# Optimization experiments

Hardware: AMD Instinct MI355X
Metric: run time of the kernel (lower is better)

Reference implementation:

```python
import jax, jax.numpy as jnp
import numpy as np

EMBED = 1024
HEADS = 16
HEAD_DIM = EMBED // HEADS
WIN = 256  # attention_window w; band width = 2w+1


def setup_inputs() -> dict:
    key = jax.random.key(0)
    ks = jax.random.split(key, 10)
    b, s, e = 2, 4096, EMBED
    scale = 1.0 / np.sqrt(e)
    inp = {"x": jax.random.normal(ks[0], (b, s, e), jnp.float32)}
    for i, (wn, bn) in enumerate([("Wq", "bq"), ("Wk", "bk"), ("Wv", "bv"), ("Wo", "bo")]):
        inp[wn] = jax.random.normal(ks[1 + i], (e, e), jnp.float32) * scale
        inp[bn] = jax.random.normal(ks[5 + i], (e,), jnp.float32) * 0.01
    return inp


def _rope_headaxis(x):
    # Replicates RotaryEmbedding applied to [b, s, h, d]: the original indexes
    # x.shape[2] (== num_heads here), so phase varies over the HEAD axis.
    h, d = x.shape[2], x.shape[3]
    inv = 1.0 / (10000.0 ** (jnp.arange(0, d, 2, dtype=jnp.float32) / d))
    freqs = jnp.arange(h, dtype=jnp.float32)[:, None] * inv[None, :]
    emb = jnp.concatenate([freqs, freqs], axis=-1)  # [h, d]
    cos = jnp.cos(emb)[None, None]  # [1,1,h,d]
    sin = jnp.sin(emb)[None, None]
    x2 = jnp.stack([-x[..., 1::2], x[..., 0::2]], axis=-1).reshape(x.shape)
    return x * cos + x2 * sin


def reference(x, Wq, bq, Wk, bk, Wv, bv, Wo, bo):
    b, s, e = x.shape
    h, d, w = HEADS, HEAD_DIM, WIN
    q = (x @ Wq.T + bq).reshape(b, s, h, d)
    k = (x @ Wk.T + bk).reshape(b, s, h, d)
    v = (x @ Wv.T + bv).reshape(b, s, h, d)
    q = _rope_headaxis(q) / jnp.sqrt(jnp.float32(d))
    k = _rope_headaxis(k)

    # Band (sliding-window) attention: query chunk c of size w attends to key
    # chunks c-1, c, c+1 (3w keys); relative-position + boundary masking makes
    # this identical to the original sliding_chunks band of width 2w+1.
    nc = s // w
    qc = q.reshape(b, nc, w, h, d)
    pad = [(0, 0), (w, w), (0, 0), (0, 0)]
    kp = jnp.pad(k, pad)
    vp = jnp.pad(v, pad)
    idx = jnp.arange(nc)[:, None] * w + jnp.arange(3 * w)[None, :]  # [nc, 3w]
    k3 = kp[:, idx]  # [b, nc, 3w, h, d]
    v3 = vp[:, idx]
    scores = jnp.einsum('bcxhd,bcyhd->bhcxy', qc, k3)  # [b,h,nc,w,3w]

    c = jnp.arange(nc)[:, None, None]
    xq = jnp.arange(w)[None, :, None]
    y = jnp.arange(3 * w)[None, None, :]
    kpos = c * w + y - w  # absolute key position
    valid = (y >= xq) & (y <= xq + 2 * w) & (kpos >= 0) & (kpos < s)
    scores = jnp.where(valid[None, None], scores, -jnp.inf)

    probs = jax.nn.softmax(scores, axis=-1)  # fp32 softmax, as in original
    ctx = jnp.einsum('bhcxy,bcyhd->bcxhd', probs, v3).reshape(b, s, e)
    return ctx @ Wo.T + bo
```

## Files before the change

### kernel.cpp

```cpp
#include <hip/hip_runtime.h>


typedef _Float16 half8 __attribute__((ext_vector_type(8)));
typedef _Float16 half4v __attribute__((ext_vector_type(4)));
typedef float floatx4 __attribute__((ext_vector_type(4)));

typedef __attribute__((address_space(3))) unsigned int lds_u32;
typedef const __attribute__((address_space(1))) unsigned int glb_u32;

__device__ __forceinline__ void async_copy16(const void* g, void* l) {
  __builtin_amdgcn_global_load_lds((glb_u32*)g, (lds_u32*)l, 16, 0, 0);
}

__global__ __launch_bounds__(256) void convert_kernel(
    const float* __restrict__ x, const float* __restrict__ wq,
    const float* __restrict__ wk, const float* __restrict__ wv,
    const float* __restrict__ wo, _Float16* __restrict__ dst) {
  const int e0 = (blockIdx.x * 256 + threadIdx.x) * 4;
  const float* src; int off;
  if      (e0 <  8388608) { src = x;  off = e0; }
  else if (e0 <  9437184) { src = wq; off = e0 -  8388608; }
  else if (e0 < 10485760) { src = wk; off = e0 -  9437184; }
  else if (e0 < 11534336) { src = wv; off = e0 - 10485760; }
  else                    { src = wo; off = e0 - 11534336; }
  const float4 f = *(const float4*)(src + off);
  half4v h;
  h[0] = (_Float16)f.x; h[1] = (_Float16)f.y;
  h[2] = (_Float16)f.z; h[3] = (_Float16)f.w;
  *(half4v*)(dst + e0) = h;
}

__global__ __launch_bounds__(256, 2) void gemm_qkv_kernel(
    const _Float16* __restrict__ A, const _Float16* __restrict__ w0,
    const _Float16* __restrict__ w1, const _Float16* __restrict__ w2,
    const float* __restrict__ b0, const float* __restrict__ b1,
    const float* __restrict__ b2, _Float16* __restrict__ o0,
    _Float16* __restrict__ o1, _Float16* __restrict__ o2) {
  __shared__ _Float16 smem[17408];
  _Float16* As = smem;
  _Float16* Bs = smem + 8192;

  const int tid = threadIdx.x;
  const int w = tid >> 6, lane = tid & 63;
  const int l4 = lane & 15, quad = lane >> 4;
  const int wm = w & 1, wn = w >> 1;

  const int bid = blockIdx.x;
  const int xcd = bid & 7, li = bid >> 3;
  const int z = li >> 6, r_ = li & 63;
  const int n_l = r_ >> 3, m_l = r_ & 7;
  const int m0 = (xcd * 8 + m_l) * 128;
  const int n0 = n_l * 128;

  const _Float16* B; const float* bias; _Float16* out;
  if (z == 0)      { B = w0; bias = b0; out = o0; }
  else if (z == 1) { B = w1; bias = b1; out = o1; }
  else             { B = w2; bias = b2; out = o2; }
  const bool dorope = z < 2;
  const float scl = (z == 0) ? 0.18033688f : 1.0f;

  const floatx4 zero = {0.f, 0.f, 0.f, 0.f};
  floatx4 acc[4][4];
#pragma unroll
  for (int i = 0; i < 4; ++i)
#pragma unroll
    for (int j = 0; j < 4; ++j) acc[i][j] = zero;

  for (int kt = 0; kt < 16; ++kt) {
    const int k0 = kt * 64;
#pragma unroll
    for (int i = 0; i < 4; ++i) {
      const int p = i * 256 + tid;
      const int r = p >> 3;
      const int c = (p & 7) ^ (r & 7);
      async_copy16(A + (m0 + r) * 1024 + k0 + c * 8, As + (i * 256 + w * 64) * 8);
      async_copy16(B + (n0 + r) * 1024 + k0 + c * 8, Bs + (i * 256 + w * 64) * 8);
    }
    __syncthreads();
#pragma unroll
    for (int ks = 0; ks < 2; ++ks) {
      half8 af[4], bf[4];
#pragma unroll
      for (int mt = 0; mt < 4; ++mt)
        af[mt] = *(const half8*)(As + (wm * 64 + mt * 16 + l4) * 64 +
                                 (((ks * 4 + quad) ^ (l4 & 7)) * 8));
#pragma unroll
      for (int nt = 0; nt < 4; ++nt)
        bf[nt] = *(const half8*)(Bs + (wn * 64 + nt * 16 + l4) * 64 +
                                 (((ks * 4 + quad) ^ (l4 & 7)) * 8));
#pragma unroll
      for (int mt = 0; mt < 4; ++mt)
#pragma unroll
        for (int nt = 0; nt < 4; ++nt)
          acc[mt][nt] = __builtin_amdgcn_mfma_f32_16x16x32_f16(af[mt], bf[nt], acc[mt][nt], 0, 0, 0);
    }
    __syncthreads();
  }

  _Float16* tile = smem;
#pragma unroll
  for (int nt = 0; nt < 4; ++nt) {
    const int n = n0 + wn * 64 + nt * 16 + l4;
    const float bval = bias[n];
    const int hh = n >> 6;
    float c_ = 1.f, ss = 0.f;
    if (dorope) {
      const float freq = __expf((float)(n & 31) * -0.28782314f);
      float s_;
      __sincosf((float)hh * freq, &s_, &c_);
      ss = (n & 1) ? s_ : -s_;
    }
#pragma unroll
    for (int mt = 0; mt < 4; ++mt)
#pragma unroll
      for (int r = 0; r < 4; ++r) {
        float val = acc[mt][nt][r] + bval;
        const float prt = __shfl_xor(val, 1);
        if (dorope) val = (val * c_ + prt * ss) * scl;
        const int ml = wm * 64 + mt * 16 + quad * 4 + r;
        const int nl = wn * 64 + nt * 16 + l4;
        if (z == 2) tile[nl * 132 + ml] = (_Float16)val;
        else        tile[ml * 132 + nl] = (_Float16)val;
      }
  }
  __syncthreads();
  if (z == 2) {
#pragma unroll
    for (int j = 0; j < 8; ++j) {
      const int idx = j * 256 + tid;
      const int row = idx >> 4, cb = idx & 15;
      const int n = n0 + row, hh = n >> 6, dd = n & 63;
      const int m = m0 + cb * 8, bb = m >> 12, s = m & 4095;
      const half8 vals = *(const half8*)(tile + row * 132 + cb * 8);
      *(half8*)(out + (bb * 16 + hh) * 262144 + dd * 4096 + s) = vals;
    }
  } else {
#pragma unroll
    for (int j = 0; j < 8; ++j) {
      const int idx = j * 256 + tid;
      const int row = idx >> 4, cb = idx & 15;
      const int n = n0 + cb * 8, hh = n >> 6, dd = n & 63;
      const int m = m0 + row, bb = m >> 12, s = m & 4095;
      const half8 vals = *(const half8*)(tile + row * 132 + cb * 8);
      *(half8*)(out + ((bb * 16 + hh) * 4096 + s) * 64 + dd) = vals;
    }
  }
}

__global__ __launch_bounds__(256, 2) void gemm_out_kernel(
    const _Float16* __restrict__ A, const _Float16* __restrict__ B,
    const float* __restrict__ bias, float* __restrict__ out) {
  __shared__ _Float16 smem[16384];
  _Float16* As = smem;
  _Float16* Bs = smem + 8192;

  const int tid = threadIdx.x;
  const int w = tid >> 6, lane = tid & 63;
  const int l4 = lane & 15, quad = lane >> 4;
  const int wm = w & 1, wn = w >> 1;

  const int bid = blockIdx.x;
  const int xcd = bid & 7, li = bid >> 3;
  const int n_l = li >> 3, m_l = li & 7;
  const int m0 = (xcd * 8 + m_l) * 128;
  const int n0 = n_l * 128;

  const floatx4 zero = {0.f, 0.f, 0.f, 0.f};
  floatx4 acc[4][4];
#pragma unroll
  for (int i = 0; i < 4; ++i)
#pragma unroll
    for (int j = 0; j < 4; ++j) acc[i][j] = zero;

  for (int kt = 0; kt < 16; ++kt) {
    const int k0 = kt * 64;
#pragma unroll
    for (int i = 0; i < 4; ++i) {
      const int p = i * 256 + tid;
      const int r = p >> 3;
      const int c = (p & 7) ^ (r & 7);
      async_copy16(A + (m0 + r) * 1024 + k0 + c * 8, As + (i * 256 + w * 64) * 8);
      async_copy16(B + (n0 + r) * 1024 + k0 + c * 8, Bs + (i * 256 + w * 64) * 8);
    }
    __syncthreads();
#pragma unroll
    for (int ks = 0; ks < 2; ++ks) {
      half8 af[4], bf[4];
#pragma unroll
      for (int mt = 0; mt < 4; ++mt)
        af[mt] = *(const half8*)(As + (wm * 64 + mt * 16 + l4) * 64 +
                                 (((ks * 4 + quad) ^ (l4 & 7)) * 8));
#pragma unroll
      for (int nt = 0; nt < 4; ++nt)
        bf[nt] = *(const half8*)(Bs + (wn * 64 + nt * 16 + l4) * 64 +
                                 (((ks * 4 + quad) ^ (l4 & 7)) * 8));
#pragma unroll
      for (int mt = 0; mt < 4; ++mt)
#pragma unroll
        for (int nt = 0; nt < 4; ++nt)
          acc[mt][nt] = __builtin_amdgcn_mfma_f32_16x16x32_f16(af[mt], bf[nt], acc[mt][nt], 0, 0, 0);
    }
    __syncthreads();
  }

#pragma unroll
  for (int nt = 0; nt < 4; ++nt) {
    const int n = n0 + wn * 64 + nt * 16 + l4;
    const float bval = bias[n];
#pragma unroll
    for (int mt = 0; mt < 4; ++mt)
#pragma unroll
      for (int r = 0; r < 4; ++r) {
        const int m = m0 + wm * 64 + mt * 16 + quad * 4 + r;
        out[m * 1024 + n] = acc[mt][nt][r] + bval;
      }
  }
}

__global__ __launch_bounds__(256, 2) void attn_kernel(
    const _Float16* __restrict__ qg, const _Float16* __restrict__ kg,
    const _Float16* __restrict__ vtg, _Float16* __restrict__ ctx) {
  __shared__ _Float16 Ks[2][128 * 64];
  __shared__ _Float16 Vs[2][64 * 128];

  const int tid = threadIdx.x;
  const int w = tid >> 6, lane = tid & 63;
  const int l4 = lane & 15, quad = lane >> 4;

  const int bid = blockIdx.x;
  const int xcd = bid & 7, li = bid >> 3;
  const int bh = xcd * 4 + (li >> 4);
  const int q0 = (li & 15) * 256;

  const _Float16* qbh = qg + bh * 262144;
  const _Float16* kbh = kg + bh * 262144;
  const _Float16* vbh = vtg + bh * 262144;

  half8 qf[2][2][2];
#pragma unroll
  for (int sub = 0; sub < 2; ++sub)
#pragma unroll
    for (int nt = 0; nt < 2; ++nt)
#pragma unroll
      for (int ks = 0; ks < 2; ++ks)
        qf[sub][nt][ks] = *(const half8*)(qbh + (q0 + sub * 128 + w * 32 + nt * 16 + l4) * 64 +
                                          ks * 32 + quad * 8);

  const floatx4 zero = {0.f, 0.f, 0.f, 0.f};
  floatx4 OT[2][4][2];
  float l_st[2][2];
#pragma unroll
  for (int sub = 0; sub < 2; ++sub) {
#pragma unroll
    for (int md = 0; md < 4; ++md)
#pragma unroll
      for (int nt = 0; nt < 2; ++nt) OT[sub][md][nt] = zero;
#pragma unroll
    for (int nt = 0; nt < 2; ++nt) l_st[sub][nt] = 0.f;
  }

  const int tb = (q0 == 0) ? 2 : 0;
  const int te = (q0 == 3840) ? 3 : 5;

  auto stage = [&](int b_, int kv0_) {
#pragma unroll
    for (int i = 0; i < 4; ++i) {
      const int p = i * 256 + tid;
      const int rk = p >> 3, ck = (p & 7) ^ (rk & 7);
      async_copy16(kbh + (kv0_ + rk) * 64 + ck * 8, &Ks[b_][(i * 256 + w * 64) * 8]);
      const int rv = p >> 4, cv = (p & 15) ^ (rv & 7);
      async_copy16(vbh + rv * 4096 + kv0_ + cv * 8, &Vs[b_][(i * 256 + w * 64) * 8]);
    }
  };

  stage(tb & 1, q0 - 256 + tb * 128);

  for (int t = tb; t <= te; ++t) {
    const int kv0 = q0 - 256 + t * 128;
    if (t < te) {
      stage((t + 1) & 1, kv0 + 128);
      asm volatile("s_waitcnt vmcnt(8)" ::: "memory");
    } else {
      asm volatile("s_waitcnt vmcnt(0)" ::: "memory");
    }
    __builtin_amdgcn_s_barrier();
    const _Float16* Kc = Ks[t & 1];
    const _Float16* Vc = Vs[t & 1];

#pragma unroll
    for (int sub = 0; sub < 2; ++sub) {
      const int qbase = q0 + sub * 128 + w * 32;
#pragma unroll
      for (int hf = 0; hf < 2; ++hf) {
        const int kb = hf * 64;
        const int k_lo = kv0 + kb, k_hi = k_lo + 63;
        if (k_lo - (qbase + 31) > 256 || k_hi - qbase < -256) continue;
        const bool needm = (k_lo - (qbase + 31) < -256) || (k_hi - qbase > 256);

        floatx4 ST[4][2];
#pragma unroll
        for (int m = 0; m < 4; ++m)
#pragma unroll
          for (int nt = 0; nt < 2; ++nt) ST[m][nt] = zero;
#pragma unroll
        for (int ks = 0; ks < 2; ++ks)
#pragma unroll
          for (int m = 0; m < 4; ++m) {
            const half8 kf = *(const half8*)(Kc + (kb + m * 16 + l4) * 64 +
                                             ((ks * 4 + quad) ^ (l4 & 7)) * 8);
#pragma unroll
            for (int nt = 0; nt < 2; ++nt)
              ST[m][nt] = __builtin_amdgcn_mfma_f32_16x16x32_f16(kf, qf[sub][nt][ks], ST[m][nt], 0, 0, 0);
          }

        if (needm) {
#pragma unroll
          for (int m = 0; m < 4; ++m)
#pragma unroll
            for (int r = 0; r < 4; ++r) {
              const int key = kv0 + kb + m * 16 + quad * 4 + r;
#pragma unroll
              for (int nt = 0; nt < 2; ++nt) {
                const int d = key - (qbase + nt * 16 + l4);
                if (d < -256 || d > 256) ST[m][nt][r] = -1e30f;
              }
            }
        }

#pragma unroll
        for (int nt = 0; nt < 2; ++nt) {
          float rs = 0.f;
#pragma unroll
          for (int m = 0; m < 4; ++m)
#pragma unroll
            for (int r = 0; r < 4; ++r) {
              const float pv = exp2f(ST[m][nt][r] - 4.0f);
              ST[m][nt][r] = pv;
              rs += pv;
            }
          l_st[sub][nt] += rs;
        }

#pragma unroll
        for (int m = 0; m < 4; ++m) {
          half4v pb[2];
#pragma unroll
          for (int nt = 0; nt < 2; ++nt) {
            const auto lo = __builtin_amdgcn_cvt_pkrtz(ST[m][nt][0], ST[m][nt][1]);
            const auto hi = __builtin_amdgcn_cvt_pkrtz(ST[m][nt][2], ST[m][nt][3]);
            pb[nt][0] = (_Float16)lo[0]; pb[nt][1] = (_Float16)lo[1];
            pb[nt][2] = (_Float16)hi[0]; pb[nt][3] = (_Float16)hi[1];
          }
#pragma unroll
          for (int md = 0; md < 4; ++md) {
            const half4v vf = *(const half4v*)(Vc + (md * 16 + l4) * 128 +
                                               (((hf * 8 + m * 2 + (quad >> 1)) ^ (l4 & 7)) * 8 +
                                                (quad & 1) * 4));
#pragma unroll
            for (int nt = 0; nt < 2; ++nt)
              OT[sub][md][nt] = __builtin_amdgcn_mfma_f32_16x16x16f16(vf, pb[nt], OT[sub][md][nt], 0, 0, 0);
          }
        }
      }
    }

    if (t < te) {
      asm volatile("s_waitcnt lgkmcnt(0)" ::: "memory");
      __builtin_amdgcn_sched_barrier(0);
      __builtin_amdgcn_s_barrier();
    }
  }

  const int b = bh >> 4, hh = bh & 15;
#pragma unroll
  for (int sub = 0; sub < 2; ++sub)
#pragma unroll
    for (int nt = 0; nt < 2; ++nt) {
      float lt = l_st[sub][nt];
      lt += __shfl_xor(lt, 16);
      lt += __shfl_xor(lt, 32);
      const float inv_l = 1.f / lt;
      const int s = q0 + sub * 128 + w * 32 + nt * 16 + l4;
#pragma unroll
      for (int md = 0; md < 4; ++md) {
        half4v o;
#pragma unroll
        for (int r = 0; r < 4; ++r) o[r] = (_Float16)(OT[sub][md][nt][r] * inv_l);
        *(half4v*)(ctx + (b * 4096 + s) * 1024 + hh * 64 + md * 16 + quad * 4) = o;
      }
    }
}

extern "C" void kernel_launch(void* const* d_in, const int* in_sizes, int n_in,
                              void* d_out, int out_size, void* d_ws, size_t ws_size,
                              hipStream_t stream) {
  const float* x  = (const float*)d_in[0];
  const float* Wq = (const float*)d_in[1];
  const float* bq = (const float*)d_in[2];
  const float* Wk = (const float*)d_in[3];
  const float* bk = (const float*)d_in[4];
  const float* Wv = (const float*)d_in[5];
  const float* bv = (const float*)d_in[6];
  const float* Wo = (const float*)d_in[7];
  const float* bo = (const float*)d_in[8];

  _Float16* ws   = (_Float16*)d_ws;
  _Float16* xh   = ws;
  _Float16* wqh  = ws + 8388608;
  _Float16* wkh  = ws + 9437184;
  _Float16* wvh  = ws + 10485760;
  _Float16* woh  = ws + 11534336;
  _Float16* qh   = ws + 12582912;
  _Float16* kh   = ws + 20971520;
  _Float16* vth  = ws + 29360128;
  _Float16* ctxh = xh;

  convert_kernel<<<12288, 256, 0, stream>>>(x, Wq, Wk, Wv, Wo, ws);
  gemm_qkv_kernel<<<1536, 256, 0, stream>>>(xh, wqh, wkh, wvh,
                                            bq, bk, bv, qh, kh, vth);
  attn_kernel<<<512, 256, 0, stream>>>(qh, kh, vth, ctxh);
  gemm_out_kernel<<<512, 256, 0, stream>>>(ctxh, woh, bo, (float*)d_out);
}
```

Measured before the change: 227.9 us.

## Double-buffer GEMM K-tiles with async LDS prefetch in QKV and output projections

Both projection GEMMs now use two LDS buffers with a K-tile of 32 instead of a single buffer with a K-tile of 64. The next tile's global-to-LDS async copies are issued before computing the current one, and a partial vmcnt wait lets loads overlap the MFMA work. The swizzle is adjusted for the narrower 32-wide rows, and per-thread offsets are hoisted out of the loop. In exchange the loop runs twice as many iterations with two barriers each, and each iteration does less MFMA work per barrier.

```diff
diff --git a/kernel.cpp b/kernel.cpp
--- a/kernel.cpp
+++ b/kernel.cpp
@@ -37,8 +37,6 @@
     const float* __restrict__ b2, _Float16* __restrict__ o0,
     _Float16* __restrict__ o1, _Float16* __restrict__ o2) {
   __shared__ _Float16 smem[17408];
-  _Float16* As = smem;
-  _Float16* Bs = smem + 8192;
 
   const int tid = threadIdx.x;
   const int w = tid >> 6, lane = tid & 63;
@@ -59,6 +57,28 @@
   const bool dorope = z < 2;
   const float scl = (z == 0) ? 0.18033688f : 1.0f;
 
+  int aoff[2], boff[2];
+#pragma unroll
+  for (int i = 0; i < 2; ++i) {
+    const int p = i * 256 + tid;
+    const int r = p >> 2;
+    const int c = (p & 3) ^ (r & 3) ^ ((r >> 2) & 1);
+    aoff[i] = (m0 + r) * 1024 + c * 8;
+    boff[i] = (n0 + r) * 1024 + c * 8;
+  }
+  const int ldst = w * 512;
+
+  auto stage = [&](int b_, int kt) {
+    _Float16* Ad = smem + b_ * 8192;
+    _Float16* Bd = Ad + 4096;
+    const int k0 = kt * 32;
+#pragma unroll
+    for (int i = 0; i < 2; ++i) {
+      async_copy16(A + aoff[i] + k0, Ad + i * 2048 + ldst);
+      async_copy16(B + boff[i] + k0, Bd + i * 2048 + ldst);
+    }
+  };
+
   const floatx4 zero = {0.f, 0.f, 0.f, 0.f};
   floatx4 acc[4][4];
 #pragma unroll
@@ -66,35 +86,34 @@
 #pragma unroll
     for (int j = 0; j < 4; ++j) acc[i][j] = zero;
 
-  for (int kt = 0; kt < 16; ++kt) {
-    const int k0 = kt * 64;
-#pragma unroll
-    for (int i = 0; i < 4; ++i) {
-      const int p = i * 256 + tid;
-      const int r = p >> 3;
-      const int c = (p & 7) ^ (r & 7);
-      async_copy16(A + (m0 + r) * 1024 + k0 + c * 8, As + (i * 256 + w * 64) * 8);
-      async_copy16(B + (n0 + r) * 1024 + k0 + c * 8, Bs + (i * 256 + w * 64) * 8);
-    }
-    __syncthreads();
-#pragma unroll
-    for (int ks = 0; ks < 2; ++ks) {
-      half8 af[4], bf[4];
-#pragma unroll
-      for (int mt = 0; mt < 4; ++mt)
-        af[mt] = *(const half8*)(As + (wm * 64 + mt * 16 + l4) * 64 +
-                                 (((ks * 4 + quad) ^ (l4 & 7)) * 8));
+  const int slot = (quad ^ (l4 & 3) ^ ((l4 >> 2) & 1)) * 8;
+
+  stage(0, 0);
+  for (int kt = 0; kt < 32; ++kt) {
+    if (kt < 31) {
+      stage((kt + 1) & 1, kt + 1);
+      asm volatile("s_waitcnt vmcnt(4)" ::: "memory");
+    } else {
+      asm volatile("s_waitcnt vmcnt(0)" ::: "memory");
+    }
+    __builtin_amdgcn_s_barrier();
+    const _Float16* As = smem + (kt & 1) * 8192;
+    const _Float16* Bs = As + 4096;
+    half8 af[4], bf[4];
+#pragma unroll
+    for (int mt = 0; mt < 4; ++mt)
+      af[mt] = *(const half8*)(As + (wm * 64 + mt * 16 + l4) * 32 + slot);
+#pragma unroll
+    for (int nt = 0; nt < 4; ++nt)
+      bf[nt] = *(const half8*)(Bs + (wn * 64 + nt * 16 + l4) * 32 + slot);
+#pragma unroll
+    for (int mt = 0; mt < 4; ++mt)
 #pragma unroll
       for (int nt = 0; nt < 4; ++nt)
-        bf[nt] = *(const half8*)(Bs + (wn * 64 + nt * 16 + l4) * 64 +
-                                 (((ks * 4 + quad) ^ (l4 & 7)) * 8));
-#pragma unroll
-      for (int mt = 0; mt < 4; ++mt)
-#pragma unroll
-        for (int nt = 0; nt < 4; ++nt)
-          acc[mt][nt] = __builtin_amdgcn_mfma_f32_16x16x32_f16(af[mt], bf[nt], acc[mt][nt], 0, 0, 0);
-    }
-    __syncthreads();
+        acc[mt][nt] = __builtin_amdgcn_mfma_f32_16x16x32_f16(af[mt], bf[nt], acc[mt][nt], 0, 0, 0);
+    asm volatile("s_waitcnt lgkmcnt(0)" ::: "memory");
+    __builtin_amdgcn_sched_barrier(0);
+    __builtin_amdgcn_s_barrier();
   }
 
   _Float16* tile = smem;
@@ -151,8 +170,6 @@
     const _Float16* __restrict__ A, const _Float16* __restrict__ B,
     const float* __restrict__ bias, float* __restrict__ out) {
   __shared__ _Float16 smem[16384];
-  _Float16* As = smem;
-  _Float16* Bs = smem + 8192;
 
   const int tid = threadIdx.x;
   const int w = tid >> 6, lane = tid & 63;
@@ -165,6 +182,28 @@
   const int m0 = (xcd * 8 + m_l) * 128;
   const int n0 = n_l * 128;
 
+  int aoff[2], boff[2];
+#pragma unroll
+  for (int i = 0; i < 2; ++i) {
+    const int p = i * 256 + tid;
+    const int r = p >> 2;
+    const int c = (p & 3) ^ (r & 3) ^ ((r >> 2) & 1);
+    aoff[i] = (m0 + r) * 1024 + c * 8;
+    boff[i] = (n0 + r) * 1024 + c * 8;
+  }
+  const int ldst = w * 512;
+
+  auto stage = [&](int b_, int kt) {
+    _Float16* Ad = smem + b_ * 8192;
+    _Float16* Bd = Ad + 4096;
+    const int k0 = kt * 32;
+#pragma unroll
+    for (int i = 0; i < 2; ++i) {
+      async_copy16(A + aoff[i] + k0, Ad + i * 2048 + ldst);
+      async_copy16(B + boff[i] + k0, Bd + i * 2048 + ldst);
+    }
+  };
+
   const floatx4 zero = {0.f, 0.f, 0.f, 0.f};
   floatx4 acc[4][4];
 #pragma unroll
@@ -172,35 +211,34 @@
 #pragma unroll
     for (int j = 0; j < 4; ++j) acc[i][j] = zero;
 
-  for (int kt = 0; kt < 16; ++kt) {
-    const int k0 = kt * 64;
-#pragma unroll
-    for (int i = 0; i < 4; ++i) {
-      const int p = i * 256 + tid;
-      const int r = p >> 3;
-      const int c = (p & 7) ^ (r & 7);
-      async_copy16(A + (m0 + r) * 1024 + k0 + c * 8, As + (i * 256 + w * 64) * 8);
-      async_copy16(B + (n0 + r) * 1024 + k0 + c * 8, Bs + (i * 256 + w * 64) * 8);
-    }
-    __syncthreads();
-#pragma unroll
-    for (int ks = 0; ks < 2; ++ks) {
-      half8 af[4], bf[4];
-#pragma unroll
-      for (int mt = 0; mt < 4; ++mt)
-        af[mt] = *(const half8*)(As + (wm * 64 + mt * 16 + l4) * 64 +
-                                 (((ks * 4 + quad) ^ (l4 & 7)) * 8));
+  const int slot = (quad ^ (l4 & 3) ^ ((l4 >> 2) & 1)) * 8;
+
+  stage(0, 0);
+  for (int kt = 0; kt < 32; ++kt) {
+    if (kt < 31) {
+      stage((kt + 1) & 1, kt + 1);
+      asm volatile("s_waitcnt vmcnt(4)" ::: "memory");
+    } else {
+      asm volatile("s_waitcnt vmcnt(0)" ::: "memory");
+    }
+    __builtin_amdgcn_s_barrier();
+    const _Float16* As = smem + (kt & 1) * 8192;
+    const _Float16* Bs = As + 4096;
+    half8 af[4], bf[4];
+#pragma unroll
+    for (int mt = 0; mt < 4; ++mt)
+      af[mt] = *(const half8*)(As + (wm * 64 + mt * 16 + l4) * 32 + slot);
+#pragma unroll
+    for (int nt = 0; nt < 4; ++nt)
+      bf[nt] = *(const half8*)(Bs + (wn * 64 + nt * 16 + l4) * 32 + slot);
+#pragma unroll
+    for (int mt = 0; mt < 4; ++mt)
 #pragma unroll
       for (int nt = 0; nt < 4; ++nt)
-        bf[nt] = *(const half8*)(Bs + (wn * 64 + nt * 16 + l4) * 64 +
-                                 (((ks * 4 + quad) ^ (l4 & 7)) * 8));
-#pragma unroll
-      for (int mt = 0; mt < 4; ++mt)
-#pragma unroll
-        for (int nt = 0; nt < 4; ++nt)
-          acc[mt][nt] = __builtin_amdgcn_mfma_f32_16x16x32_f16(af[mt], bf[nt], acc[mt][nt], 0, 0, 0);
-    }
-    __syncthreads();
+        acc[mt][nt] = __builtin_amdgcn_mfma_f32_16x16x32_f16(af[mt], bf[nt], acc[mt][nt], 0, 0, 0);
+    asm volatile("s_waitcnt lgkmcnt(0)" ::: "memory");
+    __builtin_amdgcn_sched_barrier(0);
+    __builtin_amdgcn_s_barrier();
   }
 
 #pragma unroll
```

New measurement: 236.1 us. 1.04x slower.

## Double-buffer LDS tiles in QKV and output GEMMs with async prefetch

Applied to the files above, without the earlier changes.

Both GEMM kernels now use two LDS buffers. Each iteration issues the global-to-LDS async copies for the next K tile before computing on the current one, and waits with a partial vmcnt so loads overlap the MFMAs. Address offsets are precomputed once per thread, and __syncthreads is replaced by explicit waitcnt plus s_barrier. LDS per block grows to 64KB, which could limit occupancy at two blocks per CU, and the hand-written waitcnt counts must match the number of outstanding loads.

```diff
diff --git a/kernel.cpp b/kernel.cpp
--- a/kernel.cpp
+++ b/kernel.cpp
@@ -36,9 +36,7 @@
     const float* __restrict__ b0, const float* __restrict__ b1,
     const float* __restrict__ b2, _Float16* __restrict__ o0,
     _Float16* __restrict__ o1, _Float16* __restrict__ o2) {
-  __shared__ _Float16 smem[17408];
-  _Float16* As = smem;
-  _Float16* Bs = smem + 8192;
+  __shared__ _Float16 smem[32768];
 
   const int tid = threadIdx.x;
   const int w = tid >> 6, lane = tid & 63;
@@ -59,6 +57,28 @@
   const bool dorope = z < 2;
   const float scl = (z == 0) ? 0.18033688f : 1.0f;
 
+  int aoff[4], boff[4];
+#pragma unroll
+  for (int i = 0; i < 4; ++i) {
+    const int p = i * 256 + tid;
+    const int r = p >> 3;
+    const int c = (p & 7) ^ (r & 7);
+    aoff[i] = (m0 + r) * 1024 + c * 8;
+    boff[i] = (n0 + r) * 1024 + c * 8;
+  }
+  const int ldst = (w * 64) * 8;
+
+  auto stage = [&](int b_, int kt) {
+    _Float16* Ad = smem + b_ * 16384;
+    _Float16* Bd = Ad + 8192;
+    const int k0 = kt * 64;
+#pragma unroll
+    for (int i = 0; i < 4; ++i) {
+      async_copy16(A + aoff[i] + k0, Ad + i * 2048 + ldst);
+      async_copy16(B + boff[i] + k0, Bd + i * 2048 + ldst);
+    }
+  };
+
   const floatx4 zero = {0.f, 0.f, 0.f, 0.f};
   floatx4 acc[4][4];
 #pragma unroll
@@ -66,17 +86,17 @@
 #pragma unroll
     for (int j = 0; j < 4; ++j) acc[i][j] = zero;
 
+  stage(0, 0);
   for (int kt = 0; kt < 16; ++kt) {
-    const int k0 = kt * 64;
-#pragma unroll
-    for (int i = 0; i < 4; ++i) {
-      const int p = i * 256 + tid;
-      const int r = p >> 3;
-      const int c = (p & 7) ^ (r & 7);
-      async_copy16(A + (m0 + r) * 1024 + k0 + c * 8, As + (i * 256 + w * 64) * 8);
-      async_copy16(B + (n0 + r) * 1024 + k0 + c * 8, Bs + (i * 256 + w * 64) * 8);
-    }
-    __syncthreads();
+    if (kt < 15) {
+      stage((kt + 1) & 1, kt + 1);
+      asm volatile("s_waitcnt vmcnt(8)" ::: "memory");
+    } else {
+      asm volatile("s_waitcnt vmcnt(0)" ::: "memory");
+    }
+    __builtin_amdgcn_s_barrier();
+    const _Float16* As = smem + (kt & 1) * 16384;
+    const _Float16* Bs = As + 8192;
 #pragma unroll
     for (int ks = 0; ks < 2; ++ks) {
       half8 af[4], bf[4];
@@ -94,7 +114,9 @@
         for (int nt = 0; nt < 4; ++nt)
           acc[mt][nt] = __builtin_amdgcn_mfma_f32_16x16x32_f16(af[mt], bf[nt], acc[mt][nt], 0, 0, 0);
     }
-    __syncthreads();
+    asm volatile("s_waitcnt lgkmcnt(0)" ::: "memory");
+    __builtin_amdgcn_sched_barrier(0);
+    __builtin_amdgcn_s_barrier();
   }
 
   _Float16* tile = smem;
@@ -150,9 +172,7 @@
 __global__ __launch_bounds__(256, 2) void gemm_out_kernel(
     const _Float16* __restrict__ A, const _Float16* __restrict__ B,
     const float* __restrict__ bias, float* __restrict__ out) {
-  __shared__ _Float16 smem[16384];
-  _Float16* As = smem;
-  _Float16* Bs = smem + 8192;
+  __shared__ _Float16 smem[32768];
 
   const int tid = threadIdx.x;
   const int w = tid >> 6, lane = tid & 63;
@@ -165,6 +185,28 @@
   const int m0 = (xcd * 8 + m_l) * 128;
   const int n0 = n_l * 128;
 
+  int aoff[4], boff[4];
+#pragma unroll
+  for (int i = 0; i < 4; ++i) {
+    const int p = i * 256 + tid;
+    const int r = p >> 3;
+    const int c = (p & 7) ^ (r & 7);
+    aoff[i] = (m0 + r) * 1024 + c * 8;
+    boff[i] = (n0 + r) * 1024 + c * 8;
+  }
+  const int ldst = (w * 64) * 8;
+
+  auto stage = [&](int b_, int kt) {
+    _Float16* Ad = smem + b_ * 16384;
+    _Float16* Bd = Ad + 8192;
+    const int k0 = kt * 64;
+#pragma unroll
+    for (int i = 0; i < 4; ++i) {
+      async_copy16(A + aoff[i] + k0, Ad + i * 2048 + ldst);
+      async_copy16(B + boff[i] + k0, Bd + i * 2048 + ldst);
+    }
+  };
+
   const floatx4 zero = {0.f, 0.f, 0.f, 0.f};
   floatx4 acc[4][4];
 #pragma unroll
@@ -172,17 +214,17 @@
 #pragma unroll
     for (int j = 0; j < 4; ++j) acc[i][j] = zero;
 
+  stage(0, 0);
   for (int kt = 0; kt < 16; ++kt) {
-    const int k0 = kt * 64;
-#pragma unroll
-    for (int i = 0; i < 4; ++i) {
-      const int p = i * 256 + tid;
-      const int r = p >> 3;
-      const int c = (p & 7) ^ (r & 7);
-      async_copy16(A + (m0 + r) * 1024 + k0 + c * 8, As + (i * 256 + w * 64) * 8);
-      async_copy16(B + (n0 + r) * 1024 + k0 + c * 8, Bs + (i * 256 + w * 64) * 8);
-    }
-    __syncthreads();
+    if (kt < 15) {
+      stage((kt + 1) & 1, kt + 1);
+      asm volatile("s_waitcnt vmcnt(8)" ::: "memory");
+    } else {
+      asm volatile("s_waitcnt vmcnt(0)" ::: "memory");
+    }
+    __builtin_amdgcn_s_barrier();
+    const _Float16* As = smem + (kt & 1) * 16384;
+    const _Float16* Bs = As + 8192;
 #pragma unroll
     for (int ks = 0; ks < 2; ++ks) {
       half8 af[4], bf[4];
@@ -200,7 +242,9 @@
         for (int nt = 0; nt < 4; ++nt)
           acc[mt][nt] = __builtin_amdgcn_mfma_f32_16x16x32_f16(af[mt], bf[nt], acc[mt][nt], 0, 0, 0);
     }
-    __syncthreads();
+    asm volatile("s_waitcnt lgkmcnt(0)" ::: "memory");
+    __builtin_amdgcn_sched_barrier(0);
+    __builtin_amdgcn_s_barrier();
   }
 
 #pragma unroll
```

Result: slower. 233.9 us (+2.6%).

## Use 256x128 tiles with 8 waves and a triple-buffered async GEMM mainloop

Applied to the files above, without the earlier changes.

Both GEMMs now share a mainloop with 512-thread blocks computing 256x128 tiles and three LDS stages. Global-to-LDS async copies for tile k+2 are interleaved with the MFMA work, using explicit vmcnt waits, barriers and raised wave priority around the MFMAs. The goal is to hide memory latency and cut per-K-step sync overhead compared with the single-buffered load-sync-compute loop. In exchange each block uses 144KB of LDS, so occupancy drops to one block per CU, and the QKV epilogue now writes its tile in two halves.

```diff
diff --git a/kernel.cpp b/kernel.cpp
--- a/kernel.cpp
+++ b/kernel.cpp
@@ -30,27 +30,121 @@
   *(half4v*)(dst + e0) = h;
 }
 
-__global__ __launch_bounds__(256, 2) void gemm_qkv_kernel(
+__device__ __forceinline__ void mainloop_8ph(
+    const _Float16* __restrict__ A, const _Float16* __restrict__ B,
+    _Float16* smem, const int m0, const int n0, floatx4 (&acc)[4][4]) {
+  const int tid = threadIdx.x;
+  const int w = tid >> 6, lane = tid & 63;
+  const int l4 = lane & 15, quad = lane >> 4;
+  const int wm = w >> 1, wn = w & 1;
+
+  int asrc[4], bsrc[2];
+#pragma unroll
+  for (int i = 0; i < 4; ++i) {
+    const int p = i * 512 + tid;
+    const int r = p >> 3, c = (p & 7) ^ (r & 7);
+    asrc[i] = (m0 + r) * 1024 + c * 8;
+  }
+#pragma unroll
+  for (int i = 0; i < 2; ++i) {
+    const int p = i * 512 + tid;
+    const int r = p >> 3, c = (p & 7) ^ (r & 7);
+    bsrc[i] = (n0 + r) * 1024 + c * 8;
+  }
+  const int dl = w * 512;
+
+  const int arow = (wm * 64 + l4) * 64;
+  const int brow = (wn * 64 + l4) * 64;
+
+#pragma unroll
+  for (int i = 0; i < 4; ++i)
+#pragma unroll
+    for (int j = 0; j < 4; ++j) acc[i][j] = (floatx4){0.f, 0.f, 0.f, 0.f};
+
+  auto stage_full = [&](int bufbase, int kt) {
+    _Float16* Ad = smem + bufbase;
+    _Float16* Bd = Ad + 16384;
+    const int k0 = kt * 64;
+#pragma unroll
+    for (int i = 0; i < 4; ++i) async_copy16(A + asrc[i] + k0, Ad + i * 4096 + dl);
+#pragma unroll
+    for (int i = 0; i < 2; ++i) async_copy16(B + bsrc[i] + k0, Bd + i * 4096 + dl);
+  };
+
+  stage_full(0, 0);
+  stage_full(24576, 1);
+  asm volatile("s_waitcnt vmcnt(6)" ::: "memory");
+  __builtin_amdgcn_s_barrier();
+
+  int cb = 0, pb = 49152;
+  for (int T = 0; T < 16; ++T) {
+    const _Float16* As = smem + cb;
+    const _Float16* Bs = As + 16384;
+    const bool pf = (T + 2) < 16;
+    _Float16* Ad = smem + pb;
+    _Float16* Bd = Ad + 16384;
+    const int k2 = (T + 2) * 64;
+
+#pragma unroll
+    for (int ks = 0; ks < 2; ++ks) {
+      half8 af[4], bf[4];
+      const int ch = ((ks * 4 + quad) ^ (l4 & 7)) * 8;
+#pragma unroll
+      for (int mt = 0; mt < 4; ++mt)
+        af[mt] = *(const half8*)(As + arow + mt * 1024 + ch);
+#pragma unroll
+      for (int nt = 0; nt < 4; ++nt)
+        bf[nt] = *(const half8*)(Bs + brow + nt * 1024 + ch);
+      if (pf) {
+        if (ks == 0) {
+          async_copy16(A + asrc[0] + k2, Ad + dl);
+          async_copy16(A + asrc[1] + k2, Ad + 4096 + dl);
+          async_copy16(B + bsrc[0] + k2, Bd + dl);
+        } else {
+          async_copy16(A + asrc[2] + k2, Ad + 8192 + dl);
+          async_copy16(A + asrc[3] + k2, Ad + 12288 + dl);
+          async_copy16(B + bsrc[1] + k2, Bd + 4096 + dl);
+        }
+      }
+      __builtin_amdgcn_s_barrier();
+      asm volatile("s_waitcnt lgkmcnt(0)" ::: "memory");
+      __builtin_amdgcn_sched_barrier(0);
+      __builtin_amdgcn_s_setprio(1);
+#pragma unroll
+      for (int mt = 0; mt < 4; ++mt)
+#pragma unroll
+        for (int nt = 0; nt < 4; ++nt)
+          acc[mt][nt] = __builtin_amdgcn_mfma_f32_16x16x32_f16(af[mt], bf[nt], acc[mt][nt], 0, 0, 0);
+      __builtin_amdgcn_s_setprio(0);
+      if (ks == 1) {
+        if (T < 14) asm volatile("s_waitcnt vmcnt(6)" ::: "memory");
+        else        asm volatile("s_waitcnt vmcnt(0)" ::: "memory");
+      }
+      __builtin_amdgcn_s_barrier();
+    }
+    cb += 24576; if (cb == 73728) cb = 0;
+    pb += 24576; if (pb == 73728) pb = 0;
+  }
+}
+
+__global__ __launch_bounds__(512) void gemm_qkv_kernel(
     const _Float16* __restrict__ A, const _Float16* __restrict__ w0,
     const _Float16* __restrict__ w1, const _Float16* __restrict__ w2,
     const float* __restrict__ b0, const float* __restrict__ b1,
     const float* __restrict__ b2, _Float16* __restrict__ o0,
     _Float16* __restrict__ o1, _Float16* __restrict__ o2) {
-  __shared__ _Float16 smem[17408];
-  _Float16* As = smem;
-  _Float16* Bs = smem + 8192;
+  __shared__ _Float16 smem[73728];
 
   const int tid = threadIdx.x;
   const int w = tid >> 6, lane = tid & 63;
   const int l4 = lane & 15, quad = lane >> 4;
-  const int wm = w & 1, wn = w >> 1;
+  const int wm = w >> 1, wn = w & 1;
 
   const int bid = blockIdx.x;
   const int xcd = bid & 7, li = bid >> 3;
-  const int z = li >> 6, r_ = li & 63;
-  const int n_l = r_ >> 3, m_l = r_ & 7;
-  const int m0 = (xcd * 8 + m_l) * 128;
-  const int n0 = n_l * 128;
+  const int z = li >> 5, r_ = li & 31;
+  const int m0 = (xcd * 4 + (r_ & 3)) * 256;
+  const int n0 = (r_ >> 2) * 128;
 
   const _Float16* B; const float* bias; _Float16* out;
   if (z == 0)      { B = w0; bias = b0; out = o0; }
@@ -59,149 +153,83 @@
   const bool dorope = z < 2;
   const float scl = (z == 0) ? 0.18033688f : 1.0f;
 
-  const floatx4 zero = {0.f, 0.f, 0.f, 0.f};
   floatx4 acc[4][4];
-#pragma unroll
-  for (int i = 0; i < 4; ++i)
-#pragma unroll
-    for (int j = 0; j < 4; ++j) acc[i][j] = zero;
-
-  for (int kt = 0; kt < 16; ++kt) {
-    const int k0 = kt * 64;
-#pragma unroll
-    for (int i = 0; i < 4; ++i) {
-      const int p = i * 256 + tid;
-      const int r = p >> 3;
-      const int c = (p & 7) ^ (r & 7);
-      async_copy16(A + (m0 + r) * 1024 + k0 + c * 8, As + (i * 256 + w * 64) * 8);
-      async_copy16(B + (n0 + r) * 1024 + k0 + c * 8, Bs + (i * 256 + w * 64) * 8);
+  mainloop_8ph(A, B, smem, m0, n0, acc);
+
+  _Float16* tile = smem;
+  for (int h = 0; h < 2; ++h) {
+    if ((wm >> 1) == h) {
+#pragma unroll
+      for (int nt = 0; nt < 4; ++nt) {
+        const int n = n0 + wn * 64 + nt * 16 + l4;
+        const float bval = bias[n];
+        const int hh = n >> 6;
+        float c_ = 1.f, ss = 0.f;
+        if (dorope) {
+          const float freq = __expf((float)(n & 31) * -0.28782314f);
+          float s_;
+          __sincosf((float)hh * freq, &s_, &c_);
+          ss = (n & 1) ? s_ : -s_;
+        }
+#pragma unroll
+        for (int mt = 0; mt < 4; ++mt)
+#pragma unroll
+          for (int r = 0; r < 4; ++r) {
+            float val = acc[mt][nt][r] + bval;
+            const float prt = __shfl_xor(val, 1);
+            if (dorope) val = (val * c_ + prt * ss) * scl;
+            const int ml = (wm & 1) * 64 + mt * 16 + quad * 4 + r;
+            const int nl = wn * 64 + nt * 16 + l4;
+            if (z == 2) tile[nl * 132 + ml] = (_Float16)val;
+            else        tile[ml * 132 + nl] = (_Float16)val;
+          }
+      }
     }
     __syncthreads();
-#pragma unroll
-    for (int ks = 0; ks < 2; ++ks) {
-      half8 af[4], bf[4];
-#pragma unroll
-      for (int mt = 0; mt < 4; ++mt)
-        af[mt] = *(const half8*)(As + (wm * 64 + mt * 16 + l4) * 64 +
-                                 (((ks * 4 + quad) ^ (l4 & 7)) * 8));
-#pragma unroll
-      for (int nt = 0; nt < 4; ++nt)
-        bf[nt] = *(const half8*)(Bs + (wn * 64 + nt * 16 + l4) * 64 +
-                                 (((ks * 4 + quad) ^ (l4 & 7)) * 8));
-#pragma unroll
-      for (int mt = 0; mt < 4; ++mt)
-#pragma unroll
-        for (int nt = 0; nt < 4; ++nt)
-          acc[mt][nt] = __builtin_amdgcn_mfma_f32_16x16x32_f16(af[mt], bf[nt], acc[mt][nt], 0, 0, 0);
+    const int mg = m0 + h * 128;
+    const int bb = mg >> 12, sg = mg & 4095;
+    if (z == 2) {
+#pragma unroll
+      for (int j = 0; j < 4; ++j) {
+        const int idx = j * 512 + tid;
+        const int row = idx >> 4, cbk = idx & 15;
+        const int n = n0 + row, hh = n >> 6, dd = n & 63;
+        const int s = sg + cbk * 8;
+        const half8 vals = *(const half8*)(tile + row * 132 + cbk * 8);
+        *(half8*)(out + (bb * 16 + hh) * 262144 + dd * 4096 + s) = vals;
+      }
+    } else {
+#pragma unroll
+      for (int j = 0; j < 4; ++j) {
+        const int idx = j * 512 + tid;
+        const int row = idx >> 4, cbk = idx & 15;
+        const int n = n0 + cbk * 8, hh = n >> 6, dd = n & 63;
+        const int s = sg + row;
+        const half8 vals = *(const half8*)(tile + row * 132 + cbk * 8);
+        *(half8*)(out + ((bb * 16 + hh) * 4096 + s) * 64 + dd) = vals;
+      }
     }
     __syncthreads();
   }
-
-  _Float16* tile = smem;
-#pragma unroll
-  for (int nt = 0; nt < 4; ++nt) {
-    const int n = n0 + wn * 64 + nt * 16 + l4;
-    const float bval = bias[n];
-    const int hh = n >> 6;
-    float c_ = 1.f, ss = 0.f;
-    if (dorope) {
-      const float freq = __expf((float)(n & 31) * -0.28782314f);
-      float s_;
-      __sincosf((float)hh * freq, &s_, &c_);
-      ss = (n & 1) ? s_ : -s_;
-    }
-#pragma unroll
-    for (int mt = 0; mt < 4; ++mt)
-#pragma unroll
-      for (int r = 0; r < 4; ++r) {
-        float val = acc[mt][nt][r] + bval;
-        const float prt = __shfl_xor(val, 1);
-        if (dorope) val = (val * c_ + prt * ss) * scl;
-        const int ml = wm * 64 + mt * 16 + quad * 4 + r;
-        const int nl = wn * 64 + nt * 16 + l4;
-        if (z == 2) tile[nl * 132 + ml] = (_Float16)val;
-        else        tile[ml * 132 + nl] = (_Float16)val;
-      }
-  }
-  __syncthreads();
-  if (z == 2) {
-#pragma unroll
-    for (int j = 0; j < 8; ++j) {
-      const int idx = j * 256 + tid;
-      const int row = idx >> 4, cb = idx & 15;
-      const int n = n0 + row, hh = n >> 6, dd = n & 63;
-      const int m = m0 + cb * 8, bb = m >> 12, s = m & 4095;
-      const half8 vals = *(const half8*)(tile + row * 132 + cb * 8);
-      *(half8*)(out + (bb * 16 + hh) * 262144 + dd * 4096 + s) = vals;
-    }
-  } else {
-#pragma unroll
-    for (int j = 0; j < 8; ++j) {
-      const int idx = j * 256 + tid;
-      const int row = idx >> 4, cb = idx & 15;
-      const int n = n0 + cb * 8, hh = n >> 6, dd = n & 63;
-      const int m = m0 + row, bb = m >> 12, s = m & 4095;
-      const half8 vals = *(const half8*)(tile + row * 132 + cb * 8);
-      *(half8*)(out + ((bb * 16 + hh) * 4096 + s) * 64 + dd) = vals;
-    }
-  }
-}
-
-__global__ __launch_bounds__(256, 2) void gemm_out_kernel(
+}
+
+__global__ __launch_bounds__(512) void gemm_out_kernel(
     const _Float16* __restrict__ A, const _Float16* __restrict__ B,
     const float* __restrict__ bias, float* __restrict__ out) {
-  __shared__ _Float16 smem[16384];
-  _Float16* As = smem;
-  _Float16* Bs = smem + 8192;
+  __shared__ _Float16 smem[73728];
 
   const int tid = threadIdx.x;
   const int w = tid >> 6, lane = tid & 63;
   const int l4 = lane & 15, quad = lane >> 4;
-  const int wm = w & 1, wn = w >> 1;
+  const int wm = w >> 1, wn = w & 1;
 
   const int bid = blockIdx.x;
   const int xcd = bid & 7, li = bid >> 3;
-  const int n_l = li >> 3, m_l = li & 7;
-  const int m0 = (xcd * 8 + m_l) * 128;
-  const int n0 = n_l * 128;
-
-  const floatx4 zero = {0.f, 0.f, 0.f, 0.f};
+  const int m0 = (xcd * 4 + (li & 3)) * 256;
+  const int n0 = (li >> 2) * 128;
+
   floatx4 acc[4][4];
-#pragma unroll
-  for (int i = 0; i < 4; ++i)
-#pragma unroll
-    for (int j = 0; j < 4; ++j) acc[i][j] = zero;
-
-  for (int kt = 0; kt < 16; ++kt) {
-    const int k0 = kt * 64;
-#pragma unroll
-    for (int i = 0; i < 4; ++i) {
-      const int p = i * 256 + tid;
-      const int r = p >> 3;
-      const int c = (p & 7) ^ (r & 7);
-      async_copy16(A + (m0 + r) * 1024 + k0 + c * 8, As + (i * 256 + w * 64) * 8);
-      async_copy16(B + (n0 + r) * 1024 + k0 + c * 8, Bs + (i * 256 + w * 64) * 8);
-    }
-    __syncthreads();
-#pragma unroll
-    for (int ks = 0; ks < 2; ++ks) {
-      half8 af[4], bf[4];
-#pragma unroll
-      for (int mt = 0; mt < 4; ++mt)
-        af[mt] = *(const half8*)(As + (wm * 64 + mt * 16 + l4) * 64 +
-                                 (((ks * 4 + quad) ^ (l4 & 7)) * 8));
-#pragma unroll
-      for (int nt = 0; nt < 4; ++nt)
-        bf[nt] = *(const half8*)(Bs + (wn * 64 + nt * 16 + l4) * 64 +
-                                 (((ks * 4 + quad) ^ (l4 & 7)) * 8));
-#pragma unroll
-      for (int mt = 0; mt < 4; ++mt)
-#pragma unroll
-        for (int nt = 0; nt < 4; ++nt)
-          acc[mt][nt] = __builtin_amdgcn_mfma_f32_16x16x32_f16(af[mt], bf[nt], acc[mt][nt], 0, 0, 0);
-    }
-    __syncthreads();
-  }
+  mainloop_8ph(A, B, smem, m0, n0, acc);
 
 #pragma unroll
   for (int nt = 0; nt < 4; ++nt) {
@@ -416,8 +444,8 @@
   _Float16* ctxh = xh;
 
   convert_kernel<<<12288, 256, 0, stream>>>(x, Wq, Wk, Wv, Wo, ws);
-  gemm_qkv_kernel<<<1536, 256, 0, stream>>>(xh, wqh, wkh, wvh,
-                                            bq, bk, bv, qh, kh, vth);
+  gemm_qkv_kernel<<<768, 512, 0, stream>>>(xh, wqh, wkh, wvh,
+                                           bq, bk, bv, qh, kh, vth);
   attn_kernel<<<512, 256, 0, stream>>>(qh, kh, vth, ctxh);
-  gemm_out_kernel<<<512, 256, 0, stream>>>(ctxh, woh, bo, (float*)d_out);
-}
+  gemm_out_kernel<<<256, 512, 0, stream>>>(ctxh, woh, bo, (float*)d_out);
+}
```

After: 252.0 us. +10.6%, slower.
